# Performance work log

Hardware: AMD Instinct MI355X
Metric: run time of the kernel (lower is better)

Reference implementation:

```python
import jax, jax.numpy as jnp
import numpy as np
from jax import lax

B, T_ENCO, N_INP, N_HID, T_DECO = 1024, 128, 128, 256, 24


def _lin(x, W, b):
    return x @ W.T + b


def _lstm_cell(x, h, c, Wih, Whh, bih, bhh):
    # PyTorch LSTMCell gate order: input, forget, cell(g), output
    g = x @ Wih.T + bih + h @ Whh.T + bhh
    i, f, gg, o = jnp.split(g, 4, axis=-1)
    c2 = jax.nn.sigmoid(f) * c + jax.nn.sigmoid(i) * jnp.tanh(gg)
    return jax.nn.sigmoid(o) * jnp.tanh(c2), c2


def setup_inputs() -> dict:
    key = jax.random.key(0)
    ks = iter(jax.random.split(key, 48))
    def w(shape, s=0.05):
        return jax.random.normal(next(ks), shape, jnp.float32) * s
    m = N_HID
    return {
        "input_p_q": jax.random.normal(next(ks), (B, T_ENCO, N_INP), jnp.float32),
        "label_p": jax.random.normal(next(ks), (B, T_DECO), jnp.float32),
        "Ue_W": w((m, T_ENCO)), "Ue_b": w((m,)),
        "Ue2_W": w((m, N_INP)), "Ue2_b": w((m,)),
        "We_W": w((m, 2 * N_HID)), "We_b": w((m,)),
        "Ve_W": w((1, m)), "Ve_b": w((1,)),
        "Ud_W": w((N_HID, N_HID)), "Ud_b": w((N_HID,)),
        "Wd_W": w((N_HID, 2 * N_HID)), "Wd_b": w((N_HID,)),
        "Vd_W": w((1, N_HID)), "Vd_b": w((1,)),
        "enc_Wih": w((4 * N_HID, N_INP)), "enc_Whh": w((4 * N_HID, N_HID)),
        "enc_bih": w((4 * N_HID,)), "enc_bhh": w((4 * N_HID,)),
        "mid_Wih": w((4 * N_HID, N_HID)), "mid_Whh": w((4 * N_HID, N_HID)),
        "mid_bih": w((4 * N_HID,)), "mid_bhh": w((4 * N_HID,)),
        "dec_Wih": w((4 * N_HID, N_HID)), "dec_Whh": w((4 * N_HID, N_HID)),
        "dec_bih": w((4 * N_HID,)), "dec_bhh": w((4 * N_HID,)),
        "reg_W": w((1, N_HID)), "reg_b": w((1,)),
    }


def reference(input_p_q, label_p, Ue_W, Ue_b, Ue2_W, Ue2_b, We_W, We_b, Ve_W, Ve_b,
              Ud_W, Ud_b, Wd_W, Wd_b, Vd_W, Vd_b,
              enc_Wih, enc_Whh, enc_bih, enc_bhh,
              mid_Wih, mid_Whh, mid_bih, mid_bhh,
              dec_Wih, dec_Whh, dec_bih, dec_bhh,
              reg_W, reg_b):
    bsz = input_p_q.shape[0]
    inputs = input_p_q[:, :T_ENCO, :]                       # [B, T, n_inp]
    # Ue(inputs.transpose(1,2)) is loop-invariant: [B, n_inp, m]
    ue_x = _lin(jnp.swapaxes(inputs, 1, 2), Ue_W, Ue_b)
    z = jnp.zeros((bsz, N_HID), inputs.dtype)

    # --- spatial-attention encoder (LSTMCell over time) ---
    def enc_step(carry, x_i):                               # x_i: [B, n_inp]
        h, c = carry
        hc = _lin(jnp.concatenate([h, c], axis=1), We_W, We_b)[:, None, :]
        xi = _lin(x_i, Ue2_W, Ue2_b)[:, None, :]
        score = _lin(jnp.tanh(hc + ue_x + xi), Ve_W, Ve_b)[..., 0]  # [B, n_inp]
        a = jax.nn.softmax(score, axis=1)
        h2, c2 = _lstm_cell(x_i * a, h, c, enc_Wih, enc_Whh, enc_bih, enc_bhh)
        return (h2, c2), h2

    _, enc_hs = lax.scan(enc_step, (z, z), jnp.swapaxes(inputs, 0, 1))  # [T, B, H]

    # --- middle single-layer LSTM (zero init state) ---
    def mid_step(carry, x_t):
        h, c = carry
        h2, c2 = _lstm_cell(x_t, h, c, mid_Wih, mid_Whh, mid_bih, mid_bhh)
        return (h2, c2), h2

    _, mid = lax.scan(mid_step, (z, z), enc_hs)
    mid = jnp.swapaxes(mid, 0, 1)                            # [B, T, H]
    ud_mid = _lin(mid, Ud_W, Ud_b)                           # loop-invariant

    # --- temporal-attention decoder (note: raw (un-softmaxed) scores used in bmm,
    #     matching the original code) ---
    def dec_step(carry, _):
        hi, ci = carry
        wd = _lin(jnp.concatenate([hi, ci], axis=1), Wd_W, Wd_b)[:, None, :]
        t = _lin(jnp.tanh(wd + ud_mid), Vd_W, Vd_b)[..., 0]  # [B, T]
        dec_in = jnp.einsum('bt,bth->bh', t, mid)
        hi2, ci2 = _lstm_cell(dec_in, hi, ci, dec_Wih, dec_Whh, dec_bih, dec_bhh)
        return (hi2, ci2), hi2

    _, dec = lax.scan(dec_step, (z, z), None, length=T_DECO + 6)
    dec = jnp.swapaxes(dec, 0, 1)                            # [B, T_deco+6, H]
    out = _lin(dec, reg_W, reg_b)[..., 0]                    # [B, T_deco+6]
    return out[:, -T_DECO:]
```

## Files before the change

### kernel.cpp

```cpp
#include <hip/hip_runtime.h>


#define B_   1024
#define T_   128
#define NI_  128
#define H_   256
#define H4_  1024
#define TD_  24
#define DS_  30
#define BB   4
#define TB   1024
#define LDS_BYTES 163840u

typedef _Float16 hf_t;
typedef _Float16 half8  __attribute__((ext_vector_type(8)));
typedef _Float16 half2v __attribute__((ext_vector_type(2)));

__device__ __forceinline__ float sigm(float x) {
    return __builtin_amdgcn_rcpf(1.0f + __expf(-x));
}
__device__ __forceinline__ float tanh_f(float x) {
    float e = __expf(2.0f * x);
    return 1.0f - 2.0f * __builtin_amdgcn_rcpf(e + 1.0f);
}
__device__ __forceinline__ float fdot2f(half2v a, half2v b, float c) {
#if __has_builtin(__builtin_amdgcn_fdot2)
    return __builtin_amdgcn_fdot2(a, b, c, false);
#else
    return fmaf((float)a.x, (float)b.x, fmaf((float)a.y, (float)b.y, c));
#endif
}
__device__ __forceinline__ float dot8h(half8 w, half8 x, float acc) {
    acc = fdot2f(__builtin_shufflevector(w, w, 0, 1), __builtin_shufflevector(x, x, 0, 1), acc);
    acc = fdot2f(__builtin_shufflevector(w, w, 2, 3), __builtin_shufflevector(x, x, 2, 3), acc);
    acc = fdot2f(__builtin_shufflevector(w, w, 4, 5), __builtin_shufflevector(x, x, 4, 5), acc);
    acc = fdot2f(__builtin_shufflevector(w, w, 6, 7), __builtin_shufflevector(x, x, 6, 7), acc);
    return acc;
}
__device__ __forceinline__ hf_t nt_load_h(const hf_t* p) {
#if __has_builtin(__builtin_nontemporal_load)
    return __builtin_nontemporal_load(p);
#else
    return *p;
#endif
}
__device__ __forceinline__ void nt_store_h(hf_t v, hf_t* p) {
#if __has_builtin(__builtin_nontemporal_store)
    __builtin_nontemporal_store(v, p);
#else
    *p = v;
#endif
}

#define W_WE    0u
#define W_UE2   131072u
#define W_EWIH  163840u
#define W_EWHH  294912u
#define W_MWIH  557056u
#define W_MWHH  819200u
#define W_DWIH  1081344u
#define W_DWHH  1343488u
#define W_WD    1605632u
#define W_UD    1736704u
#define SCR_A   2097152u
#define SCR_B   35651584u

__global__ void convw_kernel(const float* __restrict__ sWE, const float* __restrict__ sUE2,
                             const float* __restrict__ sEI, const float* __restrict__ sEH,
                             const float* __restrict__ sMI, const float* __restrict__ sMH,
                             const float* __restrict__ sDI, const float* __restrict__ sDH,
                             const float* __restrict__ sWD, const float* __restrict__ sUD,
                             hf_t* __restrict__ dst) {
    const int gtid = blockIdx.x * blockDim.x + threadIdx.x;
    const int gs   = gridDim.x * blockDim.x;
    for (int n = gtid; n < 131072; n += gs) {
        int e = n & 7, q = n >> 3, k = q & 255, c = q >> 8, kq = c >> 4, i = c & 15;
        dst[W_WE + n] = (hf_t)sWE[k * 512 + kq * 128 + i * 8 + e];
    }
    for (int n = gtid; n < 32768; n += gs) {
        int e = n & 7, q = n >> 3, k = q & 255, c = q >> 8, kq = c >> 2, i = c & 3;
        dst[W_UE2 + n] = (hf_t)sUE2[k * 128 + kq * 32 + i * 8 + e];
    }
    for (int n = gtid; n < 131072; n += gs) {
        int e = n & 7, q = n >> 3, o = q & 1023, i = q >> 10;
        dst[W_EWIH + n] = (hf_t)sEI[o * 128 + i * 8 + e];
    }
    for (int n = gtid; n < 262144; n += gs) {
        int e = n & 7, q = n >> 3, o = q & 1023, i = q >> 10;
        int s = o * 256 + i * 8 + e;
        dst[W_EWHH + n] = (hf_t)sEH[s];
        dst[W_MWIH + n] = (hf_t)sMI[s];
        dst[W_MWHH + n] = (hf_t)sMH[s];
        dst[W_DWIH + n] = (hf_t)sDI[s];
        dst[W_DWHH + n] = (hf_t)sDH[s];
    }
    for (int n = gtid; n < 131072; n += gs) {
        int e = n & 7, q = n >> 3, k = q & 255, c = q >> 8, kq = c >> 4, i = c & 15;
        dst[W_WD + n] = (hf_t)sWD[k * 512 + kq * 128 + i * 8 + e];
    }
    for (int n = gtid; n < 65536; n += gs)
        dst[W_UD + n] = (hf_t)sUD[n];
}

#define O_HC    0
#define O_HM    1024
#define O_XRAW  1536
#define O_XHG   2048
#define O_HCXI  2304
#define O_VES   3328
#define O_VDS   3584
#define O_RED   3840
#define O_GBUF  4096

__global__ __launch_bounds__(TB, 4) void dsrnn_kernel(
    const float* __restrict__ inp,
    const float* __restrict__ UeW,  const float* __restrict__ Ueb,
    const float* __restrict__ Ue2b,
    const float* __restrict__ Web,
    const float* __restrict__ VeW,  const float* __restrict__ Veb,
    const float* __restrict__ Udb,
    const float* __restrict__ Wdb,
    const float* __restrict__ VdW,  const float* __restrict__ Vdb,
    const float* __restrict__ ebih, const float* __restrict__ ebhh,
    const float* __restrict__ mbih, const float* __restrict__ mbhh,
    const float* __restrict__ dbih, const float* __restrict__ dbhh,
    const float* __restrict__ rW,   const float* __restrict__ rb,
    const hf_t* __restrict__ wb,
    hf_t* __restrict__ scrA,
    hf_t* __restrict__ scrB,
    float* __restrict__ out)
{
    extern __shared__ float sm[];
    float* wk = sm;
    hf_t*  u1 = (hf_t*)(sm + 8192);

    const int tid = threadIdx.x;
    const int b0  = blockIdx.x * BB;

    hf_t*  hc   = (hf_t*)(wk + O_HC);
    hf_t*  hm   = (hf_t*)(wk + O_HM);
    float* xraw = wk + O_XRAW;
    hf_t*  xhg  = (hf_t*)(wk + O_XHG);
    float* hcxi = wk + O_HCXI;
    float* ves  = wk + O_VES;
    float* vds  = wk + O_VDS;
    float* red  = wk + O_RED;
    float* gbuf = wk + O_GBUF;
    hf_t*  dinh = (hf_t*)(wk + O_HM);

    {
        const int jj = tid & 63;
        const int kg = tid >> 6;
        for (int b = 0; b < BB; ++b) {
            const float* Xg = inp + (size_t)(b0 + b) * T_ * NI_;
            for (int jh = 0; jh < 2; ++jh) {
                __syncthreads();
                for (int i = tid; i < 128 * 64; i += TB) {
                    int t = i >> 6, j2 = i & 63;
                    wk[i] = Xg[t * NI_ + jh * 64 + j2];
                }
                __syncthreads();
                const int j = jh * 64 + jj;
                for (int k = kg * 16; k < kg * 16 + 16; ++k) {
                    const float* wrow = UeW + (size_t)k * T_;
                    float acc = Ueb[k];
#pragma unroll 4
                    for (int t = 0; t < T_; ++t) acc = fmaf(wrow[t], wk[t * 64 + jj], acc);
                    if (k < 128)
                        u1[((size_t)(b * 128) + k) * 128 + j] = (hf_t)acc;
                    else
                        nt_store_h((hf_t)acc,
                                   scrA + (((size_t)(b0 + b) * 128) + (k - 128)) * 128 + j);
                }
            }
        }
    }
    __syncthreads();
    for (int i = tid; i < 1536; i += TB) wk[i] = 0.0f;
    if (tid < 256) { ves[tid] = VeW[tid]; vds[tid] = VdW[tid]; }
    __syncthreads();

    float c_enc = 0.0f, c_mid = 0.0f;

    for (int t = 0; t < T_; ++t) {
        if (tid < 512) {
            const int b = tid >> 7, j = tid & 127;
            float v = inp[((size_t)(b0 + b) * T_ + t) * NI_ + j];
            xraw[b * NI_ + j] = v;
            xhg[b * NI_ + j]  = (hf_t)v;
        }
        __syncthreads();

        {
            const int k = tid & 255, kq = tid >> 8;
            const half8* wWE = (const half8*)(wb + W_WE)  + (size_t)(kq * 16) * 256 + k;
            const half8* wU2 = (const half8*)(wb + W_UE2) + (size_t)(kq * 4)  * 256 + k;
            float a0 = 0.f, a1 = 0.f, a2 = 0.f, a3 = 0.f;
#pragma unroll 8
            for (int i = 0; i < 16; ++i) {
                half8 w = wWE[(size_t)i * 256];
                a0 = dot8h(w, *(const half8*)&hc[0 * 512 + kq * 128 + i * 8], a0);
                a1 = dot8h(w, *(const half8*)&hc[1 * 512 + kq * 128 + i * 8], a1);
                a2 = dot8h(w, *(const half8*)&hc[2 * 512 + kq * 128 + i * 8], a2);
                a3 = dot8h(w, *(const half8*)&hc[3 * 512 + kq * 128 + i * 8], a3);
            }
#pragma unroll
            for (int i = 0; i < 4; ++i) {
                half8 w = wU2[(size_t)i * 256];
                a0 = dot8h(w, *(const half8*)&xhg[0 * 128 + kq * 32 + i * 8], a0);
                a1 = dot8h(w, *(const half8*)&xhg[1 * 128 + kq * 32 + i * 8], a1);
                a2 = dot8h(w, *(const half8*)&xhg[2 * 128 + kq * 32 + i * 8], a2);
                a3 = dot8h(w, *(const half8*)&xhg[3 * 128 + kq * 32 + i * 8], a3);
            }
            gbuf[kq * 1024 + 0 * 256 + k] = a0;
            gbuf[kq * 1024 + 1 * 256 + k] = a1;
            gbuf[kq * 1024 + 2 * 256 + k] = a2;
            gbuf[kq * 1024 + 3 * 256 + k] = a3;
        }
        __syncthreads();
        {
            const int b = tid >> 8, k = tid & 255;
            hcxi[b * 256 + k] = gbuf[b * 256 + k] + gbuf[1024 + b * 256 + k]
                              + gbuf[2048 + b * 256 + k] + gbuf[3072 + b * 256 + k]
                              + Web[k] + Ue2b[k];
        }
        __syncthreads();

        {
            const int b = tid >> 8, r = tid & 255, kh = r >> 7, j = r & 127;
            const float* hx = hcxi + b * 256 + kh * 128;
            const float* vw = ves + kh * 128;
            float acc = kh ? 0.f : Veb[0];
            if (kh == 0) {
                const hf_t* up = u1 + ((size_t)(b * 128)) * 128 + j;
#pragma unroll 8
                for (int k2 = 0; k2 < 128; ++k2) {
                    float u = (float)up[(size_t)k2 * 128];
                    acc = fmaf(vw[k2], tanh_f(hx[k2] + u), acc);
                }
            } else {
                const hf_t* up = scrA + ((size_t)(b0 + b) * 128) * 128 + j;
#pragma unroll 8
                for (int k2 = 0; k2 < 128; ++k2) {
                    float u = (float)nt_load_h(up + (size_t)k2 * 128);
                    acc = fmaf(vw[k2], tanh_f(hx[k2] + u), acc);
                }
            }
            gbuf[tid] = acc;
        }
        __syncthreads();

        if (tid < 256) {
            const int b = tid >> 6, lane = tid & 63;
            const int base = b << 8;
            float sA = gbuf[base + lane]      + gbuf[base + 128 + lane];
            float sB = gbuf[base + 64 + lane] + gbuf[base + 192 + lane];
            float m = fmaxf(sA, sB);
            for (int d = 1; d < 64; d <<= 1) m = fmaxf(m, __shfl_xor(m, d));
            float eA = __expf(sA - m), eB = __expf(sB - m);
            float ssum = eA + eB;
            for (int d = 1; d < 64; d <<= 1) ssum += __shfl_xor(ssum, d);
            float inv = 1.0f / ssum;
            xhg[b * NI_ + lane]      = (hf_t)(xraw[b * NI_ + lane] * eA * inv);
            xhg[b * NI_ + lane + 64] = (hf_t)(xraw[b * NI_ + lane + 64] * eB * inv);
        }
        __syncthreads();

        {
            const int o = tid;
            const half8* wih = (const half8*)(wb + W_EWIH) + o;
            const half8* whh = (const half8*)(wb + W_EWHH) + o;
            float bias = ebih[o] + ebhh[o];
            float a0 = bias, a1 = bias, a2 = bias, a3 = bias;
#pragma unroll 8
            for (int i = 0; i < 16; ++i) {
                half8 w = wih[(size_t)i * 1024];
                a0 = dot8h(w, *(const half8*)&xhg[0 * 128 + i * 8], a0);
                a1 = dot8h(w, *(const half8*)&xhg[1 * 128 + i * 8], a1);
                a2 = dot8h(w, *(const half8*)&xhg[2 * 128 + i * 8], a2);
                a3 = dot8h(w, *(const half8*)&xhg[3 * 128 + i * 8], a3);
            }
#pragma unroll 8
            for (int i = 0; i < 32; ++i) {
                half8 w = whh[(size_t)i * 1024];
                a0 = dot8h(w, *(const half8*)&hc[0 * 512 + i * 8], a0);
                a1 = dot8h(w, *(const half8*)&hc[1 * 512 + i * 8], a1);
                a2 = dot8h(w, *(const half8*)&hc[2 * 512 + i * 8], a2);
                a3 = dot8h(w, *(const half8*)&hc[3 * 512 + i * 8], a3);
            }
            gbuf[0 * 1024 + o] = a0; gbuf[1 * 1024 + o] = a1;
            gbuf[2 * 1024 + o] = a2; gbuf[3 * 1024 + o] = a3;
        }
        __syncthreads();

        {
            const int b = tid >> 8, k = tid & 255;
            float gi = gbuf[b * H4_ + k];
            float gf = gbuf[b * H4_ + H_ + k];
            float gg = gbuf[b * H4_ + 2 * H_ + k];
            float go = gbuf[b * H4_ + 3 * H_ + k];
            float c2 = sigm(gf) * c_enc + sigm(gi) * tanh_f(gg);
            float h2 = sigm(go) * tanh_f(c2);
            c_enc = c2;
            hc[b * 512 + k]       = (hf_t)h2;
            hc[b * 512 + 256 + k] = (hf_t)c2;
        }
        __syncthreads();

        {
            const int o = tid;
            const half8* wih = (const half8*)(wb + W_MWIH) + o;
            const half8* whh = (const half8*)(wb + W_MWHH) + o;
            float bias = mbih[o] + mbhh[o];
            float a0 = bias, a1 = bias, a2 = bias, a3 = bias;
#pragma unroll 8
            for (int i = 0; i < 32; ++i) {
                half8 w = wih[(size_t)i * 1024];
                a0 = dot8h(w, *(const half8*)&hc[0 * 512 + i * 8], a0);
                a1 = dot8h(w, *(const half8*)&hc[1 * 512 + i * 8], a1);
                a2 = dot8h(w, *(const half8*)&hc[2 * 512 + i * 8], a2);
                a3 = dot8h(w, *(const half8*)&hc[3 * 512 + i * 8], a3);
            }
#pragma unroll 8
            for (int i = 0; i < 32; ++i) {
                half8 w = whh[(size_t)i * 1024];
                a0 = dot8h(w, *(const half8*)&hm[0 * 256 + i * 8], a0);
                a1 = dot8h(w, *(const half8*)&hm[1 * 256 + i * 8], a1);
                a2 = dot8h(w, *(const half8*)&hm[2 * 256 + i * 8], a2);
                a3 = dot8h(w, *(const half8*)&hm[3 * 256 + i * 8], a3);
            }
            gbuf[0 * 1024 + o] = a0; gbuf[1 * 1024 + o] = a1;
            gbuf[2 * 1024 + o] = a2; gbuf[3 * 1024 + o] = a3;
        }
        __syncthreads();

        {
            const int b = tid >> 8, k = tid & 255;
            float gi = gbuf[b * H4_ + k];
            float gf = gbuf[b * H4_ + H_ + k];
            float gg = gbuf[b * H4_ + 2 * H_ + k];
            float go = gbuf[b * H4_ + 3 * H_ + k];
            float c2 = sigm(gf) * c_mid + sigm(gi) * tanh_f(gg);
            float h2 = sigm(go) * tanh_f(c2);
            c_mid = c2;
            hm[b * 256 + k] = (hf_t)h2;
            scrB[((size_t)(b0 + b) * T_ + t) * H_ + k] = (hf_t)h2;
        }
        __syncthreads();
    }

    {
        const int b = tid >> 8, r = tid & 255, oh = r >> 7, tt = r & 127;
        const half8* mrow = (const half8*)(scrB + ((size_t)(b0 + b) * T_ + tt) * H_);
        const half8* udw = (const half8*)(wb + W_UD);
        for (int o2 = 0; o2 < 128; ++o2) {
            const int o = oh * 128 + o2;
            const half8* ur = udw + (size_t)o * 32;
            float acc = Udb[o];
#pragma unroll 8
            for (int i = 0; i < 32; ++i) acc = dot8h(ur[i], mrow[i], acc);
            if (oh == 0)
                u1[((size_t)(b * 128) + o) * 128 + tt] = (hf_t)acc;
            else
                nt_store_h((hf_t)acc,
                           scrA + (((size_t)(b0 + b) * 128) + o2) * 128 + tt);
        }
    }
    __syncthreads();
    for (int i = tid; i < 1024; i += TB) wk[i] = 0.0f;
    __syncthreads();

    float c_dec = 0.0f;

    for (int s = 0; s < DS_; ++s) {
        {
            const int k = tid & 255, kq = tid >> 8;
            const half8* wWD = (const half8*)(wb + W_WD) + (size_t)(kq * 16) * 256 + k;
            float a0 = 0.f, a1 = 0.f, a2 = 0.f, a3 = 0.f;
#pragma unroll 8
            for (int i = 0; i < 16; ++i) {
                half8 w = wWD[(size_t)i * 256];
                a0 = dot8h(w, *(const half8*)&hc[0 * 512 + kq * 128 + i * 8], a0);
                a1 = dot8h(w, *(const half8*)&hc[1 * 512 + kq * 128 + i * 8], a1);
                a2 = dot8h(w, *(const half8*)&hc[2 * 512 + kq * 128 + i * 8], a2);
                a3 = dot8h(w, *(const half8*)&hc[3 * 512 + kq * 128 + i * 8], a3);
            }
            gbuf[kq * 1024 + 0 * 256 + k] = a0;
            gbuf[kq * 1024 + 1 * 256 + k] = a1;
            gbuf[kq * 1024 + 2 * 256 + k] = a2;
            gbuf[kq * 1024 + 3 * 256 + k] = a3;
        }
        __syncthreads();
        {
            const int b = tid >> 8, k = tid & 255;
            hcxi[b * 256 + k] = gbuf[b * 256 + k] + gbuf[1024 + b * 256 + k]
                              + gbuf[2048 + b * 256 + k] + gbuf[3072 + b * 256 + k]
                              + Wdb[k];
        }
        __syncthreads();

        {
            const int b = tid >> 8, r = tid & 255, kh = r >> 7, j = r & 127;
            const float* hx = hcxi + b * 256 + kh * 128;
            const float* vw = vds + kh * 128;
            float acc = kh ? 0.f : Vdb[0];
            if (kh == 0) {
                const hf_t* up = u1 + ((size_t)(b * 128)) * 128 + j;
#pragma unroll 8
                for (int k2 = 0; k2 < 128; ++k2) {
                    float u = (float)up[(size_t)k2 * 128];
                    acc = fmaf(vw[k2], tanh_f(hx[k2] + u), acc);
                }
            } else {
                const hf_t* up = scrA + ((size_t)(b0 + b) * 128) * 128 + j;
#pragma unroll 8
                for (int k2 = 0; k2 < 128; ++k2) {
                    float u = (float)nt_load_h(up + (size_t)k2 * 128);
                    acc = fmaf(vw[k2], tanh_f(hx[k2] + u), acc);
                }
            }
            gbuf[tid] = acc;
        }
        __syncthreads();
        if (tid < 512) {
            const int b = tid >> 7, j = tid & 127;
            gbuf[1024 + b * 128 + j] = gbuf[(b << 8) + j] + gbuf[(b << 8) + 128 + j];
        }
        __syncthreads();

        {
            const int b = tid >> 8, h = tid & 255;
            const hf_t* mp = scrB + (size_t)(b0 + b) * T_ * H_ + h;
            const float* sb = gbuf + 1024 + b * 128;
            float acc = 0.0f;
            for (int j = 0; j < T_; ++j)
                acc = fmaf(sb[j], (float)mp[(size_t)j * H_], acc);
            dinh[b * 256 + h] = (hf_t)acc;
        }
        __syncthreads();

        {
            const int o = tid;
            const half8* wih = (const half8*)(wb + W_DWIH) + o;
            const half8* whh = (const half8*)(wb + W_DWHH) + o;
            float bias = dbih[o] + dbhh[o];
            float a0 = bias, a1 = bias, a2 = bias, a3 = bias;
#pragma unroll 8
            for (int i = 0; i < 32; ++i) {
                half8 w = wih[(size_t)i * 1024];
                a0 = dot8h(w, *(const half8*)&dinh[0 * 256 + i * 8], a0);
                a1 = dot8h(w, *(const half8*)&dinh[1 * 256 + i * 8], a1);
                a2 = dot8h(w, *(const half8*)&dinh[2 * 256 + i * 8], a2);
                a3 = dot8h(w, *(const half8*)&dinh[3 * 256 + i * 8], a3);
            }
#pragma unroll 8
            for (int i = 0; i < 32; ++i) {
                half8 w = whh[(size_t)i * 1024];
                a0 = dot8h(w, *(const half8*)&hc[0 * 512 + i * 8], a0);
                a1 = dot8h(w, *(const half8*)&hc[1 * 512 + i * 8], a1);
                a2 = dot8h(w, *(const half8*)&hc[2 * 512 + i * 8], a2);
                a3 = dot8h(w, *(const half8*)&hc[3 * 512 + i * 8], a3);
            }
            gbuf[0 * 1024 + o] = a0; gbuf[1 * 1024 + o] = a1;
            gbuf[2 * 1024 + o] = a2; gbuf[3 * 1024 + o] = a3;
        }
        __syncthreads();

        float h2dec;
        {
            const int b = tid >> 8, k = tid & 255;
            float gi = gbuf[b * H4_ + k];
            float gf = gbuf[b * H4_ + H_ + k];
            float gg = gbuf[b * H4_ + 2 * H_ + k];
            float go = gbuf[b * H4_ + 3 * H_ + k];
            float c2 = sigm(gf) * c_dec + sigm(gi) * tanh_f(gg);
            h2dec = sigm(go) * tanh_f(c2);
            c_dec = c2;
            hc[b * 512 + k]       = (hf_t)h2dec;
            hc[b * 512 + 256 + k] = (hf_t)c2;
        }
        __syncthreads();

        if (s >= 6) {
            const int k = tid & 255;
            float p = rW[k] * h2dec;
            for (int d = 1; d < 64; d <<= 1) p += __shfl_xor(p, d);
            if ((tid & 63) == 0) red[tid >> 6] = p;
        }
        __syncthreads();
        if (s >= 6 && tid < 4) {
            float v = red[tid * 4] + red[tid * 4 + 1]
                    + red[tid * 4 + 2] + red[tid * 4 + 3] + rb[0];
            out[(size_t)(b0 + tid) * TD_ + (s - 6)] = v;
        }
        __syncthreads();
    }
}

extern "C" void kernel_launch(void* const* d_in, const int* in_sizes, int n_in,
                              void* d_out, int out_size, void* d_ws, size_t ws_size,
                              hipStream_t stream) {
    const float* inp  = (const float*)d_in[0];
    const float* UeW  = (const float*)d_in[2];
    const float* Ueb  = (const float*)d_in[3];
    const float* Ue2W = (const float*)d_in[4];
    const float* Ue2b = (const float*)d_in[5];
    const float* WeW  = (const float*)d_in[6];
    const float* Web  = (const float*)d_in[7];
    const float* VeW  = (const float*)d_in[8];
    const float* Veb  = (const float*)d_in[9];
    const float* UdW  = (const float*)d_in[10];
    const float* Udb  = (const float*)d_in[11];
    const float* WdW  = (const float*)d_in[12];
    const float* Wdb  = (const float*)d_in[13];
    const float* VdW  = (const float*)d_in[14];
    const float* Vdb  = (const float*)d_in[15];
    const float* eWih = (const float*)d_in[16];
    const float* eWhh = (const float*)d_in[17];
    const float* ebih = (const float*)d_in[18];
    const float* ebhh = (const float*)d_in[19];
    const float* mWih = (const float*)d_in[20];
    const float* mWhh = (const float*)d_in[21];
    const float* mbih = (const float*)d_in[22];
    const float* mbhh = (const float*)d_in[23];
    const float* dWih = (const float*)d_in[24];
    const float* dWhh = (const float*)d_in[25];
    const float* dbih = (const float*)d_in[26];
    const float* dbhh = (const float*)d_in[27];
    const float* rW   = (const float*)d_in[28];
    const float* rb   = (const float*)d_in[29];

    hf_t* wsb  = (hf_t*)d_ws;
    hf_t* scrA = wsb + SCR_A;
    hf_t* scrB = wsb + SCR_B;

    static bool attr_set = false;
    if (!attr_set) {
        hipFuncSetAttribute((const void*)dsrnn_kernel,
                            hipFuncAttributeMaxDynamicSharedMemorySize, LDS_BYTES);
        attr_set = true;
    }

    convw_kernel<<<512, 256, 0, stream>>>(WeW, Ue2W, eWih, eWhh, mWih, mWhh,
                                          dWih, dWhh, WdW, UdW, wsb);

    dsrnn_kernel<<<B_ / BB, TB, LDS_BYTES, stream>>>(
        inp, UeW, Ueb, Ue2b, Web, VeW, Veb, Udb, Wdb, VdW, Vdb,
        ebih, ebhh, mbih, mbhh, dbih, dbhh, rW, rb,
        wsb, scrA, scrB, (float*)d_out);
}
```

Before: 10.31 ms.

## Halve batch rows per block to double grid size and occupancy

Each block now handles 2 batch rows instead of 4, halving LDS use so more blocks can be resident per CU (launch bounds raised), and doubling the grid to 512 blocks. Work inside each step is repartitioned: attention scores split into four 64-wide chunks with an extra reduction, and the decoder context bmm is split across two halves of T with a follow-up sum. The Ve/Vd vectors are now read from global instead of LDS. In exchange, every block re-reads the full fp16 weight matrices for half as many rows, so weight traffic per unit of work doubles, and several gate phases leave half the threads idle.

```diff
diff --git a/kernel.cpp b/kernel.cpp
--- a/kernel.cpp
+++ b/kernel.cpp
@@ -8,9 +8,9 @@
 #define H4_  1024
 #define TD_  24
 #define DS_  30
-#define BB   4
+#define BB   2
 #define TB   1024
-#define LDS_BYTES 163840u
+#define LDS_BYTES 81920u
 
 typedef _Float16 hf_t;
 typedef _Float16 half8  __attribute__((ext_vector_type(8)));
@@ -103,16 +103,14 @@
 }
 
 #define O_HC    0
-#define O_HM    1024
-#define O_XRAW  1536
-#define O_XHG   2048
-#define O_HCXI  2304
-#define O_VES   3328
-#define O_VDS   3584
-#define O_RED   3840
-#define O_GBUF  4096
-
-__global__ __launch_bounds__(TB, 4) void dsrnn_kernel(
+#define O_HM    512
+#define O_XRAW  768
+#define O_XHG   1024
+#define O_HCXI  1152
+#define O_RED   1664
+#define O_GBUF  2048
+
+__global__ __launch_bounds__(TB, 8) void dsrnn_kernel(
     const float* __restrict__ inp,
     const float* __restrict__ UeW,  const float* __restrict__ Ueb,
     const float* __restrict__ Ue2b,
@@ -132,7 +130,7 @@
 {
     extern __shared__ float sm[];
     float* wk = sm;
-    hf_t*  u1 = (hf_t*)(sm + 8192);
+    hf_t*  u1 = (hf_t*)(sm + 4096);
 
     const int tid = threadIdx.x;
     const int b0  = blockIdx.x * BB;
@@ -142,30 +140,28 @@
     float* xraw = wk + O_XRAW;
     hf_t*  xhg  = (hf_t*)(wk + O_XHG);
     float* hcxi = wk + O_HCXI;
-    float* ves  = wk + O_VES;
-    float* vds  = wk + O_VDS;
     float* red  = wk + O_RED;
     float* gbuf = wk + O_GBUF;
     hf_t*  dinh = (hf_t*)(wk + O_HM);
 
     {
-        const int jj = tid & 63;
-        const int kg = tid >> 6;
+        const int jj = tid & 31;
+        const int kg = tid >> 5;
         for (int b = 0; b < BB; ++b) {
             const float* Xg = inp + (size_t)(b0 + b) * T_ * NI_;
-            for (int jh = 0; jh < 2; ++jh) {
+            for (int jq = 0; jq < 4; ++jq) {
                 __syncthreads();
-                for (int i = tid; i < 128 * 64; i += TB) {
-                    int t = i >> 6, j2 = i & 63;
-                    wk[i] = Xg[t * NI_ + jh * 64 + j2];
+                for (int i = tid; i < 128 * 32; i += TB) {
+                    int t = i >> 5, j2 = i & 31;
+                    wk[i] = Xg[t * NI_ + jq * 32 + j2];
                 }
                 __syncthreads();
-                const int j = jh * 64 + jj;
-                for (int k = kg * 16; k < kg * 16 + 16; ++k) {
+                const int j = jq * 32 + jj;
+                for (int k = kg * 8; k < kg * 8 + 8; ++k) {
                     const float* wrow = UeW + (size_t)k * T_;
                     float acc = Ueb[k];
 #pragma unroll 4
-                    for (int t = 0; t < T_; ++t) acc = fmaf(wrow[t], wk[t * 64 + jj], acc);
+                    for (int t = 0; t < T_; ++t) acc = fmaf(wrow[t], wk[t * 32 + jj], acc);
                     if (k < 128)
                         u1[((size_t)(b * 128) + k) * 128 + j] = (hf_t)acc;
                     else
@@ -176,14 +172,13 @@
         }
     }
     __syncthreads();
-    for (int i = tid; i < 1536; i += TB) wk[i] = 0.0f;
-    if (tid < 256) { ves[tid] = VeW[tid]; vds[tid] = VdW[tid]; }
+    for (int i = tid; i < 768; i += TB) wk[i] = 0.0f;
     __syncthreads();
 
     float c_enc = 0.0f, c_mid = 0.0f;
 
     for (int t = 0; t < T_; ++t) {
-        if (tid < 512) {
+        if (tid < 256) {
             const int b = tid >> 7, j = tid & 127;
             float v = inp[((size_t)(b0 + b) * T_ + t) * NI_ + j];
             xraw[b * NI_ + j] = v;
@@ -195,66 +190,62 @@
             const int k = tid & 255, kq = tid >> 8;
             const half8* wWE = (const half8*)(wb + W_WE)  + (size_t)(kq * 16) * 256 + k;
             const half8* wU2 = (const half8*)(wb + W_UE2) + (size_t)(kq * 4)  * 256 + k;
-            float a0 = 0.f, a1 = 0.f, a2 = 0.f, a3 = 0.f;
+            float a0 = 0.f, a1 = 0.f;
 #pragma unroll 8
             for (int i = 0; i < 16; ++i) {
                 half8 w = wWE[(size_t)i * 256];
                 a0 = dot8h(w, *(const half8*)&hc[0 * 512 + kq * 128 + i * 8], a0);
                 a1 = dot8h(w, *(const half8*)&hc[1 * 512 + kq * 128 + i * 8], a1);
-                a2 = dot8h(w, *(const half8*)&hc[2 * 512 + kq * 128 + i * 8], a2);
-                a3 = dot8h(w, *(const half8*)&hc[3 * 512 + kq * 128 + i * 8], a3);
             }
 #pragma unroll
             for (int i = 0; i < 4; ++i) {
                 half8 w = wU2[(size_t)i * 256];
                 a0 = dot8h(w, *(const half8*)&xhg[0 * 128 + kq * 32 + i * 8], a0);
                 a1 = dot8h(w, *(const half8*)&xhg[1 * 128 + kq * 32 + i * 8], a1);
-                a2 = dot8h(w, *(const half8*)&xhg[2 * 128 + kq * 32 + i * 8], a2);
-                a3 = dot8h(w, *(const half8*)&xhg[3 * 128 + kq * 32 + i * 8], a3);
-            }
-            gbuf[kq * 1024 + 0 * 256 + k] = a0;
-            gbuf[kq * 1024 + 1 * 256 + k] = a1;
-            gbuf[kq * 1024 + 2 * 256 + k] = a2;
-            gbuf[kq * 1024 + 3 * 256 + k] = a3;
-        }
-        __syncthreads();
-        {
+            }
+            gbuf[kq * 512 + 0 * 256 + k] = a0;
+            gbuf[kq * 512 + 1 * 256 + k] = a1;
+        }
+        __syncthreads();
+        if (tid < 512) {
             const int b = tid >> 8, k = tid & 255;
-            hcxi[b * 256 + k] = gbuf[b * 256 + k] + gbuf[1024 + b * 256 + k]
-                              + gbuf[2048 + b * 256 + k] + gbuf[3072 + b * 256 + k]
+            hcxi[b * 256 + k] = gbuf[b * 256 + k] + gbuf[512 + b * 256 + k]
+                              + gbuf[1024 + b * 256 + k] + gbuf[1536 + b * 256 + k]
                               + Web[k] + Ue2b[k];
         }
         __syncthreads();
 
         {
-            const int b = tid >> 8, r = tid & 255, kh = r >> 7, j = r & 127;
-            const float* hx = hcxi + b * 256 + kh * 128;
-            const float* vw = ves + kh * 128;
-            float acc = kh ? 0.f : Veb[0];
-            if (kh == 0) {
-                const hf_t* up = u1 + ((size_t)(b * 128)) * 128 + j;
-#pragma unroll 8
-                for (int k2 = 0; k2 < 128; ++k2) {
+            const int b = tid >> 9, kq = (tid >> 7) & 3, j = tid & 127;
+            const float* hx = hcxi + b * 256 + kq * 64;
+            const float* vw = VeW + kq * 64;
+            float acc = (kq == 0) ? Veb[0] : 0.f;
+            if (kq < 2) {
+                const hf_t* up = u1 + ((size_t)(b * 128 + kq * 64)) * 128 + j;
+#pragma unroll 8
+                for (int k2 = 0; k2 < 64; ++k2) {
                     float u = (float)up[(size_t)k2 * 128];
                     acc = fmaf(vw[k2], tanh_f(hx[k2] + u), acc);
                 }
             } else {
-                const hf_t* up = scrA + ((size_t)(b0 + b) * 128) * 128 + j;
-#pragma unroll 8
-                for (int k2 = 0; k2 < 128; ++k2) {
+                const hf_t* up = scrA + ((size_t)(b0 + b) * 128 + (kq - 2) * 64) * 128 + j;
+#pragma unroll 8
+                for (int k2 = 0; k2 < 64; ++k2) {
                     float u = (float)nt_load_h(up + (size_t)k2 * 128);
                     acc = fmaf(vw[k2], tanh_f(hx[k2] + u), acc);
                 }
             }
-            gbuf[tid] = acc;
-        }
-        __syncthreads();
-
-        if (tid < 256) {
+            gbuf[b * 512 + kq * 128 + j] = acc;
+        }
+        __syncthreads();
+
+        if (tid < 128) {
             const int b = tid >> 6, lane = tid & 63;
-            const int base = b << 8;
-            float sA = gbuf[base + lane]      + gbuf[base + 128 + lane];
-            float sB = gbuf[base + 64 + lane] + gbuf[base + 192 + lane];
+            const int base = b << 9;
+            float sA = gbuf[base + lane]       + gbuf[base + 128 + lane]
+                     + gbuf[base + 256 + lane] + gbuf[base + 384 + lane];
+            float sB = gbuf[base + 64 + lane]  + gbuf[base + 192 + lane]
+                     + gbuf[base + 320 + lane] + gbuf[base + 448 + lane];
             float m = fmaxf(sA, sB);
             for (int d = 1; d < 64; d <<= 1) m = fmaxf(m, __shfl_xor(m, d));
             float eA = __expf(sA - m), eB = __expf(sB - m);
@@ -271,29 +262,24 @@
             const half8* wih = (const half8*)(wb + W_EWIH) + o;
             const half8* whh = (const half8*)(wb + W_EWHH) + o;
             float bias = ebih[o] + ebhh[o];
-            float a0 = bias, a1 = bias, a2 = bias, a3 = bias;
+            float a0 = bias, a1 = bias;
 #pragma unroll 8
             for (int i = 0; i < 16; ++i) {
                 half8 w = wih[(size_t)i * 1024];
                 a0 = dot8h(w, *(const half8*)&xhg[0 * 128 + i * 8], a0);
                 a1 = dot8h(w, *(const half8*)&xhg[1 * 128 + i * 8], a1);
-                a2 = dot8h(w, *(const half8*)&xhg[2 * 128 + i * 8], a2);
-                a3 = dot8h(w, *(const half8*)&xhg[3 * 128 + i * 8], a3);
             }
 #pragma unroll 8
             for (int i = 0; i < 32; ++i) {
                 half8 w = whh[(size_t)i * 1024];
                 a0 = dot8h(w, *(const half8*)&hc[0 * 512 + i * 8], a0);
                 a1 = dot8h(w, *(const half8*)&hc[1 * 512 + i * 8], a1);
-                a2 = dot8h(w, *(const half8*)&hc[2 * 512 + i * 8], a2);
-                a3 = dot8h(w, *(const half8*)&hc[3 * 512 + i * 8], a3);
             }
             gbuf[0 * 1024 + o] = a0; gbuf[1 * 1024 + o] = a1;
-            gbuf[2 * 1024 + o] = a2; gbuf[3 * 1024 + o] = a3;
-        }
-        __syncthreads();
-
-        {
+        }
+        __syncthreads();
+
+        if (tid < 512) {
             const int b = tid >> 8, k = tid & 255;
             float gi = gbuf[b * H4_ + k];
             float gf = gbuf[b * H4_ + H_ + k];
@@ -312,29 +298,24 @@
             const half8* wih = (const half8*)(wb + W_MWIH) + o;
             const half8* whh = (const half8*)(wb + W_MWHH) + o;
             float bias = mbih[o] + mbhh[o];
-            float a0 = bias, a1 = bias, a2 = bias, a3 = bias;
+            float a0 = bias, a1 = bias;
 #pragma unroll 8
             for (int i = 0; i < 32; ++i) {
                 half8 w = wih[(size_t)i * 1024];
                 a0 = dot8h(w, *(const half8*)&hc[0 * 512 + i * 8], a0);
                 a1 = dot8h(w, *(const half8*)&hc[1 * 512 + i * 8], a1);
-                a2 = dot8h(w, *(const half8*)&hc[2 * 512 + i * 8], a2);
-                a3 = dot8h(w, *(const half8*)&hc[3 * 512 + i * 8], a3);
             }
 #pragma unroll 8
             for (int i = 0; i < 32; ++i) {
                 half8 w = whh[(size_t)i * 1024];
                 a0 = dot8h(w, *(const half8*)&hm[0 * 256 + i * 8], a0);
                 a1 = dot8h(w, *(const half8*)&hm[1 * 256 + i * 8], a1);
-                a2 = dot8h(w, *(const half8*)&hm[2 * 256 + i * 8], a2);
-                a3 = dot8h(w, *(const half8*)&hm[3 * 256 + i * 8], a3);
             }
             gbuf[0 * 1024 + o] = a0; gbuf[1 * 1024 + o] = a1;
-            gbuf[2 * 1024 + o] = a2; gbuf[3 * 1024 + o] = a3;
-        }
-        __syncthreads();
-
-        {
+        }
+        __syncthreads();
+
+        if (tid < 512) {
             const int b = tid >> 8, k = tid & 255;
             float gi = gbuf[b * H4_ + k];
             float gf = gbuf[b * H4_ + H_ + k];
@@ -350,24 +331,24 @@
     }
 
     {
-        const int b = tid >> 8, r = tid & 255, oh = r >> 7, tt = r & 127;
+        const int b = tid >> 9, r = tid & 511, oq = r >> 7, tt = r & 127;
         const half8* mrow = (const half8*)(scrB + ((size_t)(b0 + b) * T_ + tt) * H_);
         const half8* udw = (const half8*)(wb + W_UD);
-        for (int o2 = 0; o2 < 128; ++o2) {
-            const int o = oh * 128 + o2;
+        for (int o2 = 0; o2 < 64; ++o2) {
+            const int o = oq * 64 + o2;
             const half8* ur = udw + (size_t)o * 32;
             float acc = Udb[o];
 #pragma unroll 8
             for (int i = 0; i < 32; ++i) acc = dot8h(ur[i], mrow[i], acc);
-            if (oh == 0)
+            if (o < 128)
                 u1[((size_t)(b * 128) + o) * 128 + tt] = (hf_t)acc;
             else
                 nt_store_h((hf_t)acc,
-                           scrA + (((size_t)(b0 + b) * 128) + o2) * 128 + tt);
+                           scrA + (((size_t)(b0 + b) * 128) + (o - 128)) * 128 + tt);
         }
     }
     __syncthreads();
-    for (int i = tid; i < 1024; i += TB) wk[i] = 0.0f;
+    for (int i = tid; i < 512; i += TB) wk[i] = 0.0f;
     __syncthreads();
 
     float c_dec = 0.0f;
@@ -376,66 +357,70 @@
         {
             const int k = tid & 255, kq = tid >> 8;
             const half8* wWD = (const half8*)(wb + W_WD) + (size_t)(kq * 16) * 256 + k;
-            float a0 = 0.f, a1 = 0.f, a2 = 0.f, a3 = 0.f;
+            float a0 = 0.f, a1 = 0.f;
 #pragma unroll 8
             for (int i = 0; i < 16; ++i) {
                 half8 w = wWD[(size_t)i * 256];
                 a0 = dot8h(w, *(const half8*)&hc[0 * 512 + kq * 128 + i * 8], a0);
                 a1 = dot8h(w, *(const half8*)&hc[1 * 512 + kq * 128 + i * 8], a1);
-                a2 = dot8h(w, *(const half8*)&hc[2 * 512 + kq * 128 + i * 8], a2);
-                a3 = dot8h(w, *(const half8*)&hc[3 * 512 + kq * 128 + i * 8], a3);
-            }
-            gbuf[kq * 1024 + 0 * 256 + k] = a0;
-            gbuf[kq * 1024 + 1 * 256 + k] = a1;
-            gbuf[kq * 1024 + 2 * 256 + k] = a2;
-            gbuf[kq * 1024 + 3 * 256 + k] = a3;
-        }
-        __syncthreads();
-        {
+            }
+            gbuf[kq * 512 + 0 * 256 + k] = a0;
+            gbuf[kq * 512 + 1 * 256 + k] = a1;
+        }
+        __syncthreads();
+        if (tid < 512) {
             const int b = tid >> 8, k = tid & 255;
-            hcxi[b * 256 + k] = gbuf[b * 256 + k] + gbuf[1024 + b * 256 + k]
-                              + gbuf[2048 + b * 256 + k] + gbuf[3072 + b * 256 + k]
+            hcxi[b * 256 + k] = gbuf[b * 256 + k] + gbuf[512 + b * 256 + k]
+                              + gbuf[1024 + b * 256 + k] + gbuf[1536 + b * 256 + k]
                               + Wdb[k];
         }
         __syncthreads();
 
         {
-            const int b = tid >> 8, r = tid & 255, kh = r >> 7, j = r & 127;
-            const float* hx = hcxi + b * 256 + kh * 128;
-            const float* vw = vds + kh * 128;
-            float acc = kh ? 0.f : Vdb[0];
-            if (kh == 0) {
-                const hf_t* up = u1 + ((size_t)(b * 128)) * 128 + j;
-#pragma unroll 8
-                for (int k2 = 0; k2 < 128; ++k2) {
+            const int b = tid >> 9, kq = (tid >> 7) & 3, j = tid & 127;
+            const float* hx = hcxi + b * 256 + kq * 64;
+            const float* vw = VdW + kq * 64;
+            float acc = (kq == 0) ? Vdb[0] : 0.f;
+            if (kq < 2) {
+                const hf_t* up = u1 + ((size_t)(b * 128 + kq * 64)) * 128 + j;
+#pragma unroll 8
+                for (int k2 = 0; k2 < 64; ++k2) {
                     float u = (float)up[(size_t)k2 * 128];
                     acc = fmaf(vw[k2], tanh_f(hx[k2] + u), acc);
                 }
             } else {
-                const hf_t* up = scrA + ((size_t)(b0 + b) * 128) * 128 + j;
-#pragma unroll 8
-                for (int k2 = 0; k2 < 128; ++k2) {
+                const hf_t* up = scrA + ((size_t)(b0 + b) * 128 + (kq - 2) * 64) * 128 + j;
+#pragma unroll 8
+                for (int k2 = 0; k2 < 64; ++k2) {
                     float u = (float)nt_load_h(up + (size_t)k2 * 128);
                     acc = fmaf(vw[k2], tanh_f(hx[k2] + u), acc);
                 }
             }
-            gbuf[tid] = acc;
+            gbuf[b * 512 + kq * 128 + j] = acc;
+        }
+        __syncthreads();
+        if (tid < 256) {
+            const int b = tid >> 7, j = tid & 127;
+            const int base = b << 9;
+            gbuf[1024 + b * 128 + j] = gbuf[base + j] + gbuf[base + 128 + j]
+                                     + gbuf[base + 256 + j] + gbuf[base + 384 + j];
+        }
+        __syncthreads();
+
+        {
+            const int b = tid >> 9, jh = (tid >> 8) & 1, h = tid & 255;
+            const hf_t* mp = scrB + (size_t)(b0 + b) * T_ * H_ + h;
+            const float* sb = gbuf + 1024 + b * 128 + jh * 64;
+            float acc = 0.0f;
+            const int jbase = jh * 64;
+            for (int j = 0; j < 64; ++j)
+                acc = fmaf(sb[j], (float)mp[(size_t)(jbase + j) * H_], acc);
+            gbuf[(b * 2 + jh) * 256 + h] = acc;
         }
         __syncthreads();
         if (tid < 512) {
-            const int b = tid >> 7, j = tid & 127;
-            gbuf[1024 + b * 128 + j] = gbuf[(b << 8) + j] + gbuf[(b << 8) + 128 + j];
-        }
-        __syncthreads();
-
-        {
             const int b = tid >> 8, h = tid & 255;
-            const hf_t* mp = scrB + (size_t)(b0 + b) * T_ * H_ + h;
-            const float* sb = gbuf + 1024 + b * 128;
-            float acc = 0.0f;
-            for (int j = 0; j < T_; ++j)
-                acc = fmaf(sb[j], (float)mp[(size_t)j * H_], acc);
-            dinh[b * 256 + h] = (hf_t)acc;
+            dinh[b * 256 + h] = (hf_t)(gbuf[b * 512 + h] + gbuf[b * 512 + 256 + h]);
         }
         __syncthreads();
 
@@ -444,30 +429,25 @@
             const half8* wih = (const half8*)(wb + W_DWIH) + o;
             const half8* whh = (const half8*)(wb + W_DWHH) + o;
             float bias = dbih[o] + dbhh[o];
-            float a0 = bias, a1 = bias, a2 = bias, a3 = bias;
+            float a0 = bias, a1 = bias;
 #pragma unroll 8
             for (int i = 0; i < 32; ++i) {
                 half8 w = wih[(size_t)i * 1024];
                 a0 = dot8h(w, *(const half8*)&dinh[0 * 256 + i * 8], a0);
                 a1 = dot8h(w, *(const half8*)&dinh[1 * 256 + i * 8], a1);
-                a2 = dot8h(w, *(const half8*)&dinh[2 * 256 + i * 8], a2);
-                a3 = dot8h(w, *(const half8*)&dinh[3 * 256 + i * 8], a3);
             }
 #pragma unroll 8
             for (int i = 0; i < 32; ++i) {
                 half8 w = whh[(size_t)i * 1024];
                 a0 = dot8h(w, *(const half8*)&hc[0 * 512 + i * 8], a0);
                 a1 = dot8h(w, *(const half8*)&hc[1 * 512 + i * 8], a1);
-                a2 = dot8h(w, *(const half8*)&hc[2 * 512 + i * 8], a2);
-                a3 = dot8h(w, *(const half8*)&hc[3 * 512 + i * 8], a3);
             }
             gbuf[0 * 1024 + o] = a0; gbuf[1 * 1024 + o] = a1;
-            gbuf[2 * 1024 + o] = a2; gbuf[3 * 1024 + o] = a3;
-        }
-        __syncthreads();
-
-        float h2dec;
-        {
+        }
+        __syncthreads();
+
+        float h2dec = 0.0f;
+        if (tid < 512) {
             const int b = tid >> 8, k = tid & 255;
             float gi = gbuf[b * H4_ + k];
             float gf = gbuf[b * H4_ + H_ + k];
@@ -481,14 +461,14 @@
         }
         __syncthreads();
 
-        if (s >= 6) {
+        if (s >= 6 && tid < 512) {
             const int k = tid & 255;
             float p = rW[k] * h2dec;
             for (int d = 1; d < 64; d <<= 1) p += __shfl_xor(p, d);
             if ((tid & 63) == 0) red[tid >> 6] = p;
         }
         __syncthreads();
-        if (s >= 6 && tid < 4) {
+        if (s >= 6 && tid < 2) {
             float v = red[tid * 4] + red[tid * 4 + 1]
                     + red[tid * 4 + 2] + red[tid * 4 + 3] + rb[0];
             out[(size_t)(b0 + tid) * TD_ + (s - 6)] = v;
```

Result: slower. 17.21 ms (+67.0%).
